# Kernel tuning notes

Measured on AMD Instinct MI355X. Metric: run time of the kernel, lower is better.

Reference implementation:

```python
import jax, jax.numpy as jnp
import numpy as np

B, S, D = 2, 2048, 1024
H, DQK, DV = 16, 64, 64

def setup_inputs() -> dict:
    key = jax.random.key(0)
    k1, k2, k3, k4, k5 = jax.random.split(key, 5)
    scale_in = 1.0 / np.sqrt(D)
    scale_v = 1.0 / np.sqrt(H * DV)
    return {
        "x":   jax.random.normal(k1, (B, S, D), dtype=jnp.float32),
        "W_q": jax.random.uniform(k2, (D, H * DQK), minval=-scale_in, maxval=scale_in, dtype=jnp.float32),
        "W_k": jax.random.uniform(k3, (D, H * DQK), minval=-scale_in, maxval=scale_in, dtype=jnp.float32),
        "W_v": jax.random.uniform(k4, (D, H * DV), minval=-scale_in, maxval=scale_in, dtype=jnp.float32),
        "W_o": jax.random.uniform(k5, (H * DV, D), minval=-scale_v, maxval=scale_v, dtype=jnp.float32),
    }

def reference(x, W_q, W_k, W_v, W_o):
    b, s, _ = x.shape
    # projections -> [B, H, S, d]
    Q = (x @ W_q).reshape(b, s, H, DQK).transpose(0, 2, 1, 3)
    K = (x @ W_k).reshape(b, s, H, DQK).transpose(0, 2, 1, 3)
    V = (x @ W_v).reshape(b, s, H, DV).transpose(0, 2, 1, 3)
    scores = jnp.einsum('bhqd,bhkd->bhqk', Q, K) / np.sqrt(DQK).astype(np.float32)
    causal_mask = jnp.triu(jnp.ones((s, s), dtype=bool), k=1)  # True above diagonal
    scores = jnp.where(causal_mask[None, None], -jnp.inf, scores)
    attn = jax.nn.softmax(scores, axis=-1)
    out = jnp.einsum('bhqk,bhkd->bhqd', attn, V)  # [B,H,S,DV]
    out = out.transpose(0, 2, 1, 3).reshape(b, s, H * DV)
    return out @ W_o
```

## Files before the change

kernel.cpp:

```cpp
#include <hip/hip_runtime.h>


typedef float  f32x4  __attribute__((ext_vector_type(4)));
typedef __bf16 bf16x8 __attribute__((ext_vector_type(8)));

__device__ __forceinline__ unsigned short f2bf(float f) {
    __bf16 h = (__bf16)f;
    return __builtin_bit_cast(unsigned short, h);
}

__device__ __forceinline__ void gld16(unsigned short* lds, const unsigned short* g) {
    __builtin_amdgcn_global_load_lds(
        (const __attribute__((address_space(1))) void*)g,
        (__attribute__((address_space(3))) void*)lds, 16, 0, 0);
}

__global__ __launch_bounds__(256) void castx(const float* __restrict__ x,
                                             unsigned short* __restrict__ xb) {
    size_t i = ((size_t)blockIdx.x * 256 + threadIdx.x) * 4;
    float4 v = *(const float4*)(x + i);
    ushort4 o;
    o.x = f2bf(v.x); o.y = f2bf(v.y); o.z = f2bf(v.z); o.w = f2bf(v.w);
    *(ushort4*)(xb + i) = o;
}

__global__ __launch_bounds__(256) void wtrans(const float* __restrict__ W0,
                                              const float* __restrict__ W1,
                                              const float* __restrict__ W2,
                                              const float* __restrict__ W3,
                                              unsigned short* __restrict__ WT) {
    __shared__ float T[64][65];
    const int z = blockIdx.z;
    const float* W = (z == 0) ? W0 : (z == 1) ? W1 : (z == 2) ? W2 : W3;
    const int k0 = blockIdx.y * 64, n0 = blockIdx.x * 64;
    const int tid = threadIdx.x;
#pragma unroll
    for (int i = 0; i < 4; i++) {
        int c = tid + i * 256;
        int r = c >> 4, col = (c & 15) * 4;
        float4 v = *(const float4*)(W + (size_t)(k0 + r) * 1024 + n0 + col);
        T[r][col] = v.x; T[r][col + 1] = v.y; T[r][col + 2] = v.z; T[r][col + 3] = v.w;
    }
    __syncthreads();
    unsigned short* out = WT + (size_t)z * 1024 * 1024;
#pragma unroll
    for (int i = 0; i < 2; i++) {
        int c = tid + i * 256;
        int nr = c >> 3, koff = (c & 7) * 8;
        union { unsigned short us[8]; uint4 v; } pk;
#pragma unroll
        for (int j = 0; j < 8; j++) pk.us[j] = f2bf(T[koff + j][nr]);
        *(uint4*)(out + (size_t)(n0 + nr) * 1024 + k0 + koff) = pk.v;
    }
}

__global__ __launch_bounds__(256) void gemm_qkv(const unsigned short* __restrict__ A,
                                                const unsigned short* __restrict__ WTall,
                                                unsigned short* __restrict__ outq,
                                                unsigned short* __restrict__ Vp) {
    __shared__ unsigned short As[128 * 64];
    __shared__ unsigned short Bs[128 * 64];
    const int tid = threadIdx.x;
    const int w = tid >> 6, lane = tid & 63, quad = lane >> 4, ln = lane & 15;

    const int blk = blockIdx.x;
    const int n0 = ((blk >> 3) & 7) * 128;
    const int g  = ((blk >> 6) << 3) | (blk & 7);
    const int z  = g >> 5;
    const int m0 = (g & 31) * 128;

    const unsigned short* BT = WTall + (size_t)z * (1024 * 1024);
    const float scl = (z == 0) ? 0.180336878f : 1.0f;
    const bool swp = (z < 2);

    const int lr8 = lane >> 3;
    const int lc8 = ((lane & 7) ^ lr8) * 8;
    const int fsw = (quad ^ (ln & 7)) * 8;

    const f32x4 z4 = {0.f, 0.f, 0.f, 0.f};
    f32x4 acc[4][4];
#pragma unroll
    for (int i = 0; i < 4; i++)
#pragma unroll
        for (int j = 0; j < 4; j++) acc[i][j] = z4;

    const int wm = (w & 1) * 64, wn = (w >> 1) * 64;
    const int Rb = w * 32;

    for (int k0 = 0; k0 < 1024; k0 += 64) {
        __syncthreads();
#pragma unroll
        for (int s = 0; s < 4; s++) {
            gld16(As + (Rb + s * 8) * 64, A  + (size_t)(m0 + Rb + s * 8 + lr8) * 1024 + k0 + lc8);
            gld16(Bs + (Rb + s * 8) * 64, BT + (size_t)(n0 + Rb + s * 8 + lr8) * 1024 + k0 + lc8);
        }
        __syncthreads();
#pragma unroll
        for (int ks = 0; ks < 2; ks++) {
            const int co = fsw ^ (ks * 32);
            bf16x8 af[4], bfr[4];
#pragma unroll
            for (int t = 0; t < 4; t++)
                af[t] = *(const bf16x8*)&As[(wm + t * 16 + ln) * 64 + co];
#pragma unroll
            for (int t = 0; t < 4; t++)
                bfr[t] = *(const bf16x8*)&Bs[(wn + t * 16 + ln) * 64 + co];
            if (swp) {
#pragma unroll
                for (int tm = 0; tm < 4; tm++)
#pragma unroll
                    for (int tn = 0; tn < 4; tn++)
                        acc[tm][tn] = __builtin_amdgcn_mfma_f32_16x16x32_bf16(
                            bfr[tn], af[tm], acc[tm][tn], 0, 0, 0);
            } else {
#pragma unroll
                for (int tm = 0; tm < 4; tm++)
#pragma unroll
                    for (int tn = 0; tn < 4; tn++)
                        acc[tm][tn] = __builtin_amdgcn_mfma_f32_16x16x32_bf16(
                            af[tm], bfr[tn], acc[tm][tn], 0, 0, 0);
            }
        }
    }

    if (swp) {
#pragma unroll
        for (int tm = 0; tm < 4; tm++)
#pragma unroll
            for (int tn = 0; tn < 4; tn++) {
                int mg = m0 + wm + tm * 16 + ln;
                int nb = n0 + wn + tn * 16 + quad * 4;
                int b = mg >> 11, s = mg & 2047, h = nb >> 6, dd = nb & 63;
                ushort4 o;
                o.x = f2bf(acc[tm][tn][0] * scl);
                o.y = f2bf(acc[tm][tn][1] * scl);
                o.z = f2bf(acc[tm][tn][2] * scl);
                o.w = f2bf(acc[tm][tn][3] * scl);
                size_t zoff = (size_t)z * (4096 * 1024);
                *(ushort4*)(outq + zoff + (((size_t)(b * 16 + h) * 2048 + s) << 6) + dd) = o;
            }
    } else {
#pragma unroll
        for (int tm = 0; tm < 4; tm++)
#pragma unroll
            for (int tn = 0; tn < 4; tn++) {
                int mg = m0 + wm + tm * 16 + quad * 4;
                int ng = n0 + wn + tn * 16 + ln;
                int b = mg >> 11, h = ng >> 6, dd = ng & 63;
                int sblk = (mg & 2047) & ~63;
                int cb = tm >> 1, t16 = tm & 1;
                int pp = cb * 32 + quad * 8 + t16 * 4;
                ushort4 o;
                o.x = f2bf(acc[tm][tn][0]);
                o.y = f2bf(acc[tm][tn][1]);
                o.z = f2bf(acc[tm][tn][2]);
                o.w = f2bf(acc[tm][tn][3]);
                *(ushort4*)(Vp + ((size_t)(b * 16 + h) * 64 + dd) * 2048 + sblk + pp) = o;
            }
    }
}

__global__ __launch_bounds__(256) void gemm_o(const unsigned short* __restrict__ A,
                                              const unsigned short* __restrict__ BT,
                                              float* __restrict__ outf) {
    __shared__ unsigned short As[128 * 64];
    __shared__ unsigned short Bs[128 * 64];
    const int tid = threadIdx.x;
    const int w = tid >> 6, lane = tid & 63, quad = lane >> 4, ln = lane & 15;

    const int blk = blockIdx.x;
    const int n0 = ((blk >> 3) & 7) * 128;
    const int m0 = (((blk >> 6) << 3) | (blk & 7)) * 128;

    const int lr8 = lane >> 3;
    const int lc8 = ((lane & 7) ^ lr8) * 8;
    const int fsw = (quad ^ (ln & 7)) * 8;

    const f32x4 z4 = {0.f, 0.f, 0.f, 0.f};
    f32x4 acc[4][4];
#pragma unroll
    for (int i = 0; i < 4; i++)
#pragma unroll
        for (int j = 0; j < 4; j++) acc[i][j] = z4;

    const int wm = (w & 1) * 64, wn = (w >> 1) * 64;
    const int Rb = w * 32;

    for (int k0 = 0; k0 < 1024; k0 += 64) {
        __syncthreads();
#pragma unroll
        for (int s = 0; s < 4; s++) {
            gld16(As + (Rb + s * 8) * 64, A  + (size_t)(m0 + Rb + s * 8 + lr8) * 1024 + k0 + lc8);
            gld16(Bs + (Rb + s * 8) * 64, BT + (size_t)(n0 + Rb + s * 8 + lr8) * 1024 + k0 + lc8);
        }
        __syncthreads();
#pragma unroll
        for (int ks = 0; ks < 2; ks++) {
            const int co = fsw ^ (ks * 32);
            bf16x8 af[4], bfr[4];
#pragma unroll
            for (int t = 0; t < 4; t++)
                af[t] = *(const bf16x8*)&As[(wm + t * 16 + ln) * 64 + co];
#pragma unroll
            for (int t = 0; t < 4; t++)
                bfr[t] = *(const bf16x8*)&Bs[(wn + t * 16 + ln) * 64 + co];
#pragma unroll
            for (int tm = 0; tm < 4; tm++)
#pragma unroll
                for (int tn = 0; tn < 4; tn++)
                    acc[tm][tn] = __builtin_amdgcn_mfma_f32_16x16x32_bf16(
                        bfr[tn], af[tm], acc[tm][tn], 0, 0, 0);
        }
    }

#pragma unroll
    for (int tm = 0; tm < 4; tm++)
#pragma unroll
        for (int tn = 0; tn < 4; tn++) {
            int mg = m0 + wm + tm * 16 + ln;
            int nb = n0 + wn + tn * 16 + quad * 4;
            *(f32x4*)(outf + (size_t)mg * 1024 + nb) = acc[tm][tn];
        }
}

__global__ __launch_bounds__(512, 4) void flash(const unsigned short* __restrict__ Qb,
                                                const unsigned short* __restrict__ Kb,
                                                const unsigned short* __restrict__ Vpb,
                                                unsigned short* __restrict__ AO) {
    __shared__ __align__(16) unsigned short Ks[2][64 * 64];
    __shared__ __align__(16) unsigned short Vs[2][64 * 64];
    const int tid = threadIdx.x, w = tid >> 6, lane = tid & 63;
    const int qd = lane >> 4, ln = lane & 15;
    const int lr = lane >> 3;
    const int lchunk = (lane & 7) ^ lr;
    const int psw = (qd ^ (ln & 7)) * 8;

    const int blk = blockIdx.x;
    const int r  = blk >> 3;
    const int qi = 15 - (r & 15);
    const int bh = ((r >> 4) << 3) | (blk & 7);
    const int qt0 = qi * 128;

    const unsigned short* Kg = Kb  + (size_t)bh * 2048 * 64;
    const unsigned short* Vg = Vpb + (size_t)bh * 64 * 2048;

    bf16x8 aq[2];
    {
        const unsigned short* Qrow = Qb + ((size_t)bh * 2048 + qt0 + w * 16 + ln) * 64 + qd * 8;
        aq[0] = *(const bf16x8*)(Qrow);
        aq[1] = *(const bf16x8*)(Qrow + 32);
    }

    const f32x4 z4 = {0.f, 0.f, 0.f, 0.f};
    f32x4 Oc[4];
#pragma unroll
    for (int td = 0; td < 4; td++) Oc[td] = z4;
    float lsum = 0.f;

    const int qrow = qt0 + w * 16 + ln;
    const int qmin = qt0 + w * 16;
    const int qmax = qmin + 15;
    const int kend = qt0 + 128;

#define FLASH_STAGE(buf, kk)                                                          \
    {                                                                                 \
        const unsigned short* kg = Kg + (size_t)((kk) + w * 8 + lr) * 64 + lchunk * 8; \
        gld16(&Ks[buf][(w * 8) * 64], kg);                                            \
        const unsigned short* vg = Vg + (size_t)(w * 8 + lr) * 2048 + (kk) + lchunk * 8; \
        gld16(&Vs[buf][(w * 8) * 64], vg);                                            \
    }

    FLASH_STAGE(0, 0);
    int cur = 0;

    for (int k0 = 0; k0 < kend; k0 += 64) {
        __syncthreads();
        if (k0 + 64 < kend) FLASH_STAGE(cur ^ 1, k0 + 64);

        if (k0 <= qmax) {
            f32x4 sc[4];
#pragma unroll
            for (int t = 0; t < 4; t++) {
                sc[t] = z4;
                if (k0 + t * 16 <= qmax) {
                    int off = (t * 16 + ln) * 64 + psw;
                    bf16x8 bk0 = *(const bf16x8*)&Ks[cur][off];
                    bf16x8 bk1 = *(const bf16x8*)&Ks[cur][off ^ 32];
                    sc[t] = __builtin_amdgcn_mfma_f32_16x16x32_bf16(bk0, aq[0], sc[t], 0, 0, 0);
                    sc[t] = __builtin_amdgcn_mfma_f32_16x16x32_bf16(bk1, aq[1], sc[t], 0, 0, 0);
                }
            }

            unsigned int pk[4][2];
#pragma unroll
            for (int t = 0; t < 4; t++) {
                if (k0 + t * 16 > qmax) { pk[t][0] = 0u; pk[t][1] = 0u; continue; }
                float e[4];
#pragma unroll
                for (int r2 = 0; r2 < 4; r2++) e[r2] = __builtin_amdgcn_exp2f(sc[t][r2]);
                if (k0 + t * 16 + 15 > qmin) {
#pragma unroll
                    for (int r2 = 0; r2 < 4; r2++)
                        if (k0 + t * 16 + qd * 4 + r2 > qrow) e[r2] = 0.f;
                }
                lsum += (e[0] + e[1]) + (e[2] + e[3]);
                pk[t][0] = (unsigned int)f2bf(e[0]) | ((unsigned int)f2bf(e[1]) << 16);
                pk[t][1] = (unsigned int)f2bf(e[2]) | ((unsigned int)f2bf(e[3]) << 16);
            }

            union { unsigned int u[4]; bf16x8 v; } apu0, apu1;
            apu0.u[0] = pk[0][0]; apu0.u[1] = pk[0][1]; apu0.u[2] = pk[1][0]; apu0.u[3] = pk[1][1];
            apu1.u[0] = pk[2][0]; apu1.u[1] = pk[2][1]; apu1.u[2] = pk[3][0]; apu1.u[3] = pk[3][1];
#pragma unroll
            for (int td = 0; td < 4; td++) {
                int voff = (td * 16 + ln) * 64 + psw;
                bf16x8 av0 = *(const bf16x8*)&Vs[cur][voff];
                bf16x8 av1 = *(const bf16x8*)&Vs[cur][voff ^ 32];
                Oc[td] = __builtin_amdgcn_mfma_f32_16x16x32_bf16(av0, apu0.v, Oc[td], 0, 0, 0);
                Oc[td] = __builtin_amdgcn_mfma_f32_16x16x32_bf16(av1, apu1.v, Oc[td], 0, 0, 0);
            }
        }
        cur ^= 1;
    }
#undef FLASH_STAGE

    lsum += __shfl_xor(lsum, 16);
    lsum += __shfl_xor(lsum, 32);
    const float inv = 1.0f / lsum;

    const int bz = bh >> 4, h = bh & 15;
    const int rowg = qt0 + w * 16 + ln;
    unsigned short* aorow = AO + ((size_t)(bz * 2048 + rowg) << 10) + h * 64 + qd * 4;
#pragma unroll
    for (int td = 0; td < 4; td++) {
        ushort4 o;
        o.x = f2bf(Oc[td][0] * inv);
        o.y = f2bf(Oc[td][1] * inv);
        o.z = f2bf(Oc[td][2] * inv);
        o.w = f2bf(Oc[td][3] * inv);
        *(ushort4*)(aorow + td * 16) = o;
    }
}

extern "C" void kernel_launch(void* const* d_in, const int* in_sizes, int n_in,
                              void* d_out, int out_size, void* d_ws, size_t ws_size,
                              hipStream_t stream) {
    const float* x  = (const float*)d_in[0];
    const float* Wq = (const float*)d_in[1];
    const float* Wk = (const float*)d_in[2];
    const float* Wv = (const float*)d_in[3];
    const float* Wo = (const float*)d_in[4];
    float* out = (float*)d_out;

    unsigned short* xb  = (unsigned short*)d_ws;
    unsigned short* WT  = xb  + (size_t)4096 * 1024;
    unsigned short* Qb  = WT  + (size_t)4 * 1024 * 1024;
    unsigned short* Kb  = Qb  + (size_t)4096 * 1024;
    unsigned short* Vb  = Kb  + (size_t)4096 * 1024;
    unsigned short* Vpb = Vb  + (size_t)4096 * 1024;
    unsigned short* AO  = Vpb + (size_t)4096 * 1024;

    castx<<<4096, 256, 0, stream>>>(x, xb);
    wtrans<<<dim3(16, 16, 4), 256, 0, stream>>>(Wq, Wk, Wv, Wo, WT);
    gemm_qkv<<<dim3(768), 256, 0, stream>>>(xb, WT, Qb, Vpb);
    flash<<<dim3(512), 512, 0, stream>>>(Qb, Kb, Vpb, AO);
    gemm_o<<<dim3(256), 256, 0, stream>>>(AO, WT + (size_t)3 * 1024 * 1024, out);
}
```

Before: 192.6 us.

## Split heavy causal query tiles across two key halves and merge partials

The flash kernel grid grows from 512 to 768 blocks. Query tiles 0–7 still run over their full causal key range. The heavier tiles 8–15 are split into two blocks, each covering half of the key range, and each writes unnormalized fp32 partial outputs and row sums into reused workspace buffers. A new merge kernel adds the two partials, normalizes them and writes bf16 into the attention output. The aim is to balance per-block work across the causal triangle and shorten the tail, at the cost of an extra launch and extra fp32 global traffic. The merge is only correct because the kernel accumulates without a running max.

After: 180.1 us. 1.07x faster.

```diff
diff --git a/kernel.cpp b/kernel.cpp
--- a/kernel.cpp
+++ b/kernel.cpp
@@ -226,7 +226,10 @@
 __global__ __launch_bounds__(512, 4) void flash(const unsigned short* __restrict__ Qb,
                                                 const unsigned short* __restrict__ Kb,
                                                 const unsigned short* __restrict__ Vpb,
-                                                unsigned short* __restrict__ AO) {
+                                                unsigned short* __restrict__ AO,
+                                                float* __restrict__ Ph0,
+                                                float* __restrict__ Ph1,
+                                                float* __restrict__ Lb) {
     __shared__ __align__(16) unsigned short Ks[2][64 * 64];
     __shared__ __align__(16) unsigned short Vs[2][64 * 64];
     const int tid = threadIdx.x, w = tid >> 6, lane = tid & 63;
@@ -236,9 +239,18 @@
     const int psw = (qd ^ (ln & 7)) * 8;
 
     const int blk = blockIdx.x;
-    const int r  = blk >> 3;
-    const int qi = 15 - (r & 15);
-    const int bh = ((r >> 4) << 3) | (blk & 7);
+    const int bh = blk & 31;
+    const int s  = blk >> 5;
+    int qi, kstart, kend, half;
+    bool heavy;
+    if (s < 8) {
+        qi = s; kstart = 0; kend = (qi + 1) * 128; half = 0; heavy = false;
+    } else {
+        int t = s - 8; half = t >> 3; qi = 15 - (t & 7); heavy = true;
+        int mid = (qi + 1) * 64;
+        kstart = half ? mid : 0;
+        kend   = half ? (qi + 1) * 128 : mid;
+    }
     const int qt0 = qi * 128;
 
     const unsigned short* Kg = Kb  + (size_t)bh * 2048 * 64;
@@ -260,7 +272,6 @@
     const int qrow = qt0 + w * 16 + ln;
     const int qmin = qt0 + w * 16;
     const int qmax = qmin + 15;
-    const int kend = qt0 + 128;
 
 #define FLASH_STAGE(buf, kk)                                                          \
     {                                                                                 \
@@ -270,10 +281,10 @@
         gld16(&Vs[buf][(w * 8) * 64], vg);                                            \
     }
 
-    FLASH_STAGE(0, 0);
+    FLASH_STAGE(0, kstart);
     int cur = 0;
 
-    for (int k0 = 0; k0 < kend; k0 += 64) {
+    for (int k0 = kstart; k0 < kend; k0 += 64) {
         __syncthreads();
         if (k0 + 64 < kend) FLASH_STAGE(cur ^ 1, k0 + 64);
 
@@ -326,20 +337,54 @@
 
     lsum += __shfl_xor(lsum, 16);
     lsum += __shfl_xor(lsum, 32);
-    const float inv = 1.0f / lsum;
-
+
+    if (!heavy) {
+        const float inv = 1.0f / lsum;
+        const int bz = bh >> 4, h = bh & 15;
+        const int rowg = qt0 + w * 16 + ln;
+        unsigned short* aorow = AO + ((size_t)(bz * 2048 + rowg) << 10) + h * 64 + qd * 4;
+#pragma unroll
+        for (int td = 0; td < 4; td++) {
+            ushort4 o;
+            o.x = f2bf(Oc[td][0] * inv);
+            o.y = f2bf(Oc[td][1] * inv);
+            o.z = f2bf(Oc[td][2] * inv);
+            o.w = f2bf(Oc[td][3] * inv);
+            *(ushort4*)(aorow + td * 16) = o;
+        }
+    } else {
+        float* P = half ? Ph1 : Ph0;
+        const int prow = ((bh * 8 + (qi - 8)) * 128) + w * 16 + ln;
+        float* Pr = P + (size_t)prow * 64 + qd * 4;
+#pragma unroll
+        for (int td = 0; td < 4; td++)
+            *(f32x4*)(Pr + td * 16) = Oc[td];
+        if (qd == 0) Lb[half * 32768 + prow] = lsum;
+    }
+}
+
+__global__ __launch_bounds__(256) void merge(const float* __restrict__ P0,
+                                             const float* __restrict__ P1,
+                                             const float* __restrict__ Lb,
+                                             unsigned short* __restrict__ AO) {
+    const int idx = blockIdx.x * 256 + threadIdx.x;
+    const int d0 = (idx & 7) * 8;
+    const int row = idx >> 3;
+    const float inv = 1.0f / (Lb[row] + Lb[32768 + row]);
+    const float* a = P0 + (size_t)row * 64 + d0;
+    const float* b = P1 + (size_t)row * 64 + d0;
+    f32x4 x0 = *(const f32x4*)a, x1 = *(const f32x4*)(a + 4);
+    f32x4 y0 = *(const f32x4*)b, y1 = *(const f32x4*)(b + 4);
+    union { unsigned short us[8]; uint4 v; } pk;
+#pragma unroll
+    for (int j = 0; j < 4; j++) {
+        pk.us[j]     = f2bf((x0[j] + y0[j]) * inv);
+        pk.us[j + 4] = f2bf((x1[j] + y1[j]) * inv);
+    }
+    const int bh = row >> 10, qi8 = (row >> 7) & 7, q = row & 127;
     const int bz = bh >> 4, h = bh & 15;
-    const int rowg = qt0 + w * 16 + ln;
-    unsigned short* aorow = AO + ((size_t)(bz * 2048 + rowg) << 10) + h * 64 + qd * 4;
-#pragma unroll
-    for (int td = 0; td < 4; td++) {
-        ushort4 o;
-        o.x = f2bf(Oc[td][0] * inv);
-        o.y = f2bf(Oc[td][1] * inv);
-        o.z = f2bf(Oc[td][2] * inv);
-        o.w = f2bf(Oc[td][3] * inv);
-        *(ushort4*)(aorow + td * 16) = o;
-    }
+    const int rowg = (qi8 + 8) * 128 + q;
+    *(uint4*)(AO + ((size_t)(bz * 2048 + rowg) << 10) + h * 64 + d0) = pk.v;
 }
 
 extern "C" void kernel_launch(void* const* d_in, const int* in_sizes, int n_in,
@@ -360,9 +405,14 @@
     unsigned short* Vpb = Vb  + (size_t)4096 * 1024;
     unsigned short* AO  = Vpb + (size_t)4096 * 1024;
 
+    float* Ph0 = (float*)Vb;
+    float* Ph1 = (float*)xb;
+    float* Lb  = (float*)WT;
+
     castx<<<4096, 256, 0, stream>>>(x, xb);
     wtrans<<<dim3(16, 16, 4), 256, 0, stream>>>(Wq, Wk, Wv, Wo, WT);
     gemm_qkv<<<dim3(768), 256, 0, stream>>>(xb, WT, Qb, Vpb);
-    flash<<<dim3(512), 512, 0, stream>>>(Qb, Kb, Vpb, AO);
+    flash<<<dim3(768), 512, 0, stream>>>(Qb, Kb, Vpb, AO, Ph0, Ph1, Lb);
+    merge<<<dim3(1024), 256, 0, stream>>>(Ph0, Ph1, Lb, AO);
     gemm_o<<<dim3(256), 256, 0, stream>>>(AO, WT + (size_t)3 * 1024 * 1024, out);
 }
```
